# Kernel tuning notes

Measured on AMD Instinct MI355X. Metric: run time of the kernel, lower is better.

Reference implementation:

```python
import jax, jax.numpy as jnp
import numpy as np
from jax import lax

B, S, T = 512, 256, 10      # batch, src len, max_len (decoder steps)
V, E, H = 28, 32, 128       # vocab, embed, hidden
PAD = 0


def setup_inputs():
    key = jax.random.key(0)
    ks = jax.random.split(key, 16)
    k = 1.0 / np.sqrt(H)

    def u(kk, shape):
        return jax.random.uniform(kk, shape, jnp.float32, -k, k)

    embed = jax.random.normal(ks[0], (V, E), jnp.float32) * 0.02
    embed = embed.at[PAD].set(0.0)  # padding_idx=0 row is zero
    return dict(
        src=jax.random.randint(ks[1], (B, S), 0, V),
        target=jax.random.randint(ks[2], (B, T), 0, V),
        embed=embed,
        # PyTorch LSTM bias b = b_ih + b_hh folded into one vector (same math)
        enc_Wih_f=u(ks[3], (4 * H, E)), enc_Whh_f=u(ks[4], (4 * H, H)), enc_b_f=u(ks[5], (4 * H,)),
        enc_Wih_b=u(ks[6], (4 * H, E)), enc_Whh_b=u(ks[7], (4 * H, H)), enc_b_b=u(ks[8], (4 * H,)),
        dec_Wih=u(ks[9], (4 * H, E)), dec_Whh=u(ks[10], (4 * H, H)), dec_b=u(ks[11], (4 * H,)),
        proj_W=u(ks[12], (H, 2 * H)), proj_b=jnp.zeros((H,), jnp.float32),
        attn_W=u(ks[13], (H, 2 * H)), attn_b=jnp.zeros((H,), jnp.float32),
        out_W=u(ks[14], (V, H)), out_b=jnp.zeros((V,), jnp.float32),
    )


def _cell(h, c, xg, Whh):
    # PyTorch LSTMCell gate order: i, f, g, o
    g = xg + h @ Whh.T
    i, f, gg, o = jnp.split(g, 4, axis=-1)
    c = jax.nn.sigmoid(f) * c + jax.nn.sigmoid(i) * jnp.tanh(gg)
    return jax.nn.sigmoid(o) * jnp.tanh(c), c


def _run_lstm(x_emb, Wih, Whh, b):
    # precompute input projections for all steps: [S, B, 4H]
    xg = jnp.einsum('bse,ge->sbg', x_emb, Wih) + b
    h0 = jnp.zeros((x_emb.shape[0], Whh.shape[1]), x_emb.dtype)

    def step(carry, xg_t):
        h, c = _cell(carry[0], carry[1], xg_t, Whh)
        return (h, c), h

    (h, c), hs = lax.scan(step, (h0, h0), xg)
    return jnp.transpose(hs, (1, 0, 2)), h, c  # [B,S,H], [B,H], [B,H]


def _forward(src, target, embed, enc_Wih_f, enc_Whh_f, enc_b_f,
             enc_Wih_b, enc_Whh_b, enc_b_b, dec_Wih, dec_Whh, dec_b,
             proj_W, proj_b, attn_W, attn_b, out_W, out_b):
    src_emb = embed[src]  # [B,S,E]
    hs_f, hf, cf = _run_lstm(src_emb, enc_Wih_f, enc_Whh_f, enc_b_f)
    hs_r, hb, cb = _run_lstm(src_emb[:, ::-1], enc_Wih_b, enc_Whh_b, enc_b_b)
    enc_out = jnp.concatenate([hs_f, hs_r[:, ::-1]], axis=-1)  # [B,S,2H]
    h0, c0 = hf + hb, cf + cb  # sum over directions (num_layers=1)
    enc_proj = jnp.einsum('bsd,hd->bsh', enc_out, proj_W) + proj_b  # [B,S,H]

    # teacher forcing with ratio=1.0: decoder input tokens = [PAD, target[:, :-1]]
    dec_tok = jnp.concatenate(
        [jnp.full((src.shape[0], 1), PAD, target.dtype), target[:, :T - 1]], axis=1)
    xg_dec = jnp.einsum('bte,ge->tbg', embed[dec_tok], dec_Wih) + dec_b  # [T,B,4H]

    def dstep(carry, xg_t):
        h, c = _cell(carry[0], carry[1], xg_t, dec_Whh)
        scores = jnp.einsum('bsh,bh->bs', enc_proj, h)
        aw = jax.nn.softmax(scores, axis=1)
        ctx = jnp.einsum('bs,bsh->bh', aw, enc_proj)
        comb = jnp.tanh(jnp.concatenate([h, ctx], axis=1) @ attn_W.T + attn_b)
        logits = comb @ out_W.T + out_b
        return (h, c), logits

    _, logits = lax.scan(dstep, (h0, c0), xg_dec)  # [T,B,V]
    return jnp.transpose(logits, (1, 0, 2))  # [B,T,V]


def reference(src, target, embed, enc_Wih_f, enc_Whh_f, enc_b_f,
              enc_Wih_b, enc_Whh_b, enc_b_b, dec_Wih, dec_Whh, dec_b,
              proj_W, proj_b, attn_W, attn_b, out_W, out_b):
    return _forward(src, target, embed, enc_Wih_f, enc_Whh_f, enc_b_f,
                    enc_Wih_b, enc_Whh_b, enc_b_b, dec_Wih, dec_Whh, dec_b,
                    proj_W, proj_b, attn_W, attn_b, out_W, out_b)
```

## Files before the change

### kernel.cpp

```cpp
#include <hip/hip_runtime.h>
#include <hip/hip_bf16.h>
#include <stdint.h>

typedef unsigned short ushort_t;
typedef unsigned int uint_t;
typedef __attribute__((ext_vector_type(8))) short bfrag;
typedef __attribute__((ext_vector_type(4))) float f32x4;

#define B_ 512
#define S_ 256
#define T_ 10
#define V_ 28
#define H_ 128

#define XTD 0
#define XTG 14336
#define WTD 43008
#define AWT 108544
#define OWT 141312
#define PWT 144896
#define WPK 177664
#define HFIN 308736
#define CFIN 439808
#define HDEC 570880
#define HS_BYTE_OFF (1226240ull * 4ull)
#define PREP_N 308736

__device__ __forceinline__ float fast_exp2(float x) { return __builtin_amdgcn_exp2f(x); }
__device__ __forceinline__ float fast_rcp(float x)  { return __builtin_amdgcn_rcpf(x); }
__device__ __forceinline__ float sigm(float x) {
    return fast_rcp(1.f + fast_exp2(-1.4426950408889634f * x));
}
__device__ __forceinline__ float tanh_(float x) {
    return 1.f - 2.f * fast_rcp(1.f + fast_exp2(2.8853900817779268f * x));
}
__device__ __forceinline__ ushort_t f2bf(float x) {
    uint_t u = __float_as_uint(x);
    return (ushort_t)((u + 0x7FFFu + ((u >> 16) & 1u)) >> 16);
}
__device__ __forceinline__ float bflo(uint_t u) { return __uint_as_float(u << 16); }
__device__ __forceinline__ float bfhi(uint_t u) { return __uint_as_float(u & 0xFFFF0000u); }

__device__ __forceinline__ void lds_barrier() {
    asm volatile("s_waitcnt lgkmcnt(0)" ::: "memory");
    __builtin_amdgcn_s_barrier();
    __builtin_amdgcn_sched_barrier(0);
}

__global__ __launch_bounds__(256) void prep_kernel(
    const float* __restrict__ embed,
    const float* __restrict__ Wih_f, const float* __restrict__ b_f,
    const float* __restrict__ Wih_b, const float* __restrict__ b_b,
    const float* __restrict__ Wih_d, const float* __restrict__ b_d,
    const float* __restrict__ Whh_f, const float* __restrict__ Whh_b,
    const float* __restrict__ Whh_d,
    const float* __restrict__ attn_W, const float* __restrict__ out_W,
    const float* __restrict__ proj_W,
    float* __restrict__ ws)
{
    int i = blockIdx.x * 256 + threadIdx.x;
    if (i < XTG) {
        int v = i >> 9, jj = i & 511;
        float acc = b_d[jj];
        #pragma unroll
        for (int e = 0; e < 32; ++e) acc = fmaf(embed[v * 32 + e], Wih_d[jj * 32 + e], acc);
        ws[XTD + i] = acc;
    } else if (i < WTD) {
        int r = i - XTG; int d = r / 14336; int rem = r % 14336;
        int v = rem >> 9, q = rem & 511;
        int uu = q >> 2, g = q & 3;
        int jj = g * 128 + uu;
        const float* Wih = d ? Wih_b : Wih_f;
        const float* bb  = d ? b_b   : b_f;
        float acc = bb[jj];
        #pragma unroll
        for (int e = 0; e < 32; ++e) acc = fmaf(embed[v * 32 + e], Wih[jj * 32 + e], acc);
        ws[XTG + r] = acc;
    } else if (i < AWT) {
        int r = i - WTD; int k = r >> 9, jj = r & 511;
        ws[WTD + r] = Whh_d[jj * 128 + k];
    } else if (i < OWT) {
        int r = i - AWT; int k = r >> 7, uu = r & 127;
        ws[i] = attn_W[uu * 256 + k];
    } else if (i < PWT) {
        int r = i - OWT; int k = r / 28, v = r % 28;
        ws[i] = out_W[v * 128 + k];
    } else if (i < WPK) {
        int r = i - PWT; int k = r >> 7, uu = r & 127;
        ws[i] = proj_W[uu * 256 + k];
    } else if (i < PREP_N) {
        int i2 = (i - WPK) * 2;
        #pragma unroll
        for (int p = 0; p < 2; ++p, ++i2) {
            int e  = i2 & 7;
            int ll = (i2 >> 3) & 63;
            int kt = (i2 >> 9) & 3;
            int ni = (i2 >> 11) & 3;
            int wv = (i2 >> 13) & 7;
            int d  = (i2 >> 16) & 1;
            int jj = (ni * 8 + wv) * 16 + (ll & 15);
            int kp = kt * 32 + ((ll >> 4) << 3) + e;
            const float* Whh = d ? Whh_b : Whh_f;
            ((ushort_t*)(ws + WPK))[i2] = f2bf(Whh[jj * 128 + kp]);
        }
    }
}

__global__ __launch_bounds__(512, 2) void enc_kernel(
    const int* __restrict__ src,
    const float* __restrict__ xtg_base,
    const ushort_t* __restrict__ wpk,
    float* __restrict__ hfin, float* __restrict__ cfin,
    ushort_t* __restrict__ hs)
{
    const int bx = blockIdx.x;
    const int dir = bx >> 7;
    const int b0 = (bx & 127) << 2;
    const int tid = threadIdx.x;
    const int w = tid >> 6, l = tid & 63;
    const int lg = l >> 4, col = l & 15;
    const int u = (w << 4) + col;
    const int row = lg;

    __shared__ __align__(16) ushort_t hb[2][4][144];
    __shared__ __align__(16) int tokl[256][4];

    for (int i = tid; i < 1024; i += 512)
        tokl[i >> 2][i & 3] = src[(b0 + (i & 3)) * S_ + (i >> 2)];
    for (int i = tid; i < 576; i += 512) ((uint_t*)hb)[i] = 0u;

    const float* xtg = xtg_base + dir * 14336;

    bfrag bf[4][4];
    {
        const ushort_t* wb = wpk + (((size_t)dir * 8 + w) << 13) + l * 8;
        #pragma unroll
        for (int ni = 0; ni < 4; ++ni)
            #pragma unroll
            for (int kt = 0; kt < 4; ++kt)
                bf[ni][kt] = *reinterpret_cast<const bfrag*>(wb + ((ni * 4 + kt) << 9));
    }
    __syncthreads();

    float c_reg = 0.f, h_reg = 0.f;

    f32x4 xg_cur, xg_next;
    {
        int p0 = dir ? (S_ - 1) : 0;
        xg_cur = *reinterpret_cast<const f32x4*>(xtg + ((size_t)tokl[p0][row] << 9) + (u << 2));
    }

    const bfrag zf = {0, 0, 0, 0, 0, 0, 0, 0};
    bfrag af0 = zf, af1 = zf, af2 = zf, af3 = zf;
    const bool ard = ((col & 3) == 0);
    const int ar = col >> 2;
    const int swz = ar << 3;
    const f32x4 zacc = {0.f, 0.f, 0.f, 0.f};

    ushort_t* hs_ptr = hs + ((size_t)(b0 + row) * S_ + (dir ? (S_ - 1) : 0)) * 256
                          + dir * 128 + u;
    const int hs_step = dir ? -256 : 256;

    for (int t = 0; t < S_; ++t) {
        const int cb = t & 1, nb = cb ^ 1;

        if (t + 1 < S_) {
            int pn = dir ? (S_ - 2 - t) : (t + 1);
            xg_next = *reinterpret_cast<const f32x4*>(xtg + ((size_t)tokl[pn][row] << 9) + (u << 2));
        }

        if (ard) {
            const ushort_t* hp = &hb[cb][ar][0];
            af0 = *reinterpret_cast<const bfrag*>(hp + ((  0 + (lg << 3)) ^ swz));
            af1 = *reinterpret_cast<const bfrag*>(hp + (( 32 + (lg << 3)) ^ swz));
            af2 = *reinterpret_cast<const bfrag*>(hp + (( 64 + (lg << 3)) ^ swz));
            af3 = *reinterpret_cast<const bfrag*>(hp + (( 96 + (lg << 3)) ^ swz));
        }

        f32x4 a0 = __builtin_amdgcn_mfma_f32_16x16x32_bf16(af0, bf[0][0], zacc, 0, 0, 0);
        f32x4 a1 = __builtin_amdgcn_mfma_f32_16x16x32_bf16(af0, bf[1][0], zacc, 0, 0, 0);
        f32x4 a2 = __builtin_amdgcn_mfma_f32_16x16x32_bf16(af0, bf[2][0], zacc, 0, 0, 0);
        f32x4 a3 = __builtin_amdgcn_mfma_f32_16x16x32_bf16(af0, bf[3][0], zacc, 0, 0, 0);
        #define KT1(AF, kt) { \
            a0 = __builtin_amdgcn_mfma_f32_16x16x32_bf16(AF, bf[0][kt], a0, 0, 0, 0); \
            a1 = __builtin_amdgcn_mfma_f32_16x16x32_bf16(AF, bf[1][kt], a1, 0, 0, 0); \
            a2 = __builtin_amdgcn_mfma_f32_16x16x32_bf16(AF, bf[2][kt], a2, 0, 0, 0); \
            a3 = __builtin_amdgcn_mfma_f32_16x16x32_bf16(AF, bf[3][kt], a3, 0, 0, 0); \
        }
        KT1(af1, 1) KT1(af2, 2) KT1(af3, 3)
        #undef KT1

        {
            float gi = a0[0] + xg_cur[0], gf = a1[0] + xg_cur[1];
            float gg = a2[0] + xg_cur[2], go = a3[0] + xg_cur[3];
            float ii = sigm(gi), ff = sigm(gf), gG = tanh_(gg), oo = sigm(go);
            c_reg = ff * c_reg + ii * gG;
            float h = oo * tanh_(c_reg);
            h_reg = h;
            ushort_t hi = f2bf(h);
            hb[nb][row][u ^ (row << 3)] = hi;
            *hs_ptr = hi;
            hs_ptr += hs_step;
        }
        xg_cur = xg_next;
        lds_barrier();
    }

    hfin[dir * 65536 + (b0 + row) * 128 + u] = h_reg;
    cfin[dir * 65536 + (b0 + row) * 128 + u] = c_reg;
}

__global__ __launch_bounds__(512, 1) void dec_lstm_kernel(
    const int* __restrict__ target,
    const float* __restrict__ xt_d,
    const float* __restrict__ WhhT_d,
    const float* __restrict__ hfin, const float* __restrict__ cfin,
    float* __restrict__ hdec)
{
    const int b0 = blockIdx.x * 2;
    const int tid = threadIdx.x;
    const int j = tid;

    __shared__ __align__(16) float h_lds[2][128];
    __shared__ __align__(16) float g_lds[2][512];

    float4 w4[32];
    #pragma unroll
    for (int kc = 0; kc < 32; ++kc) {
        w4[kc].x = WhhT_d[(kc * 4 + 0) * 512 + j];
        w4[kc].y = WhhT_d[(kc * 4 + 1) * 512 + j];
        w4[kc].z = WhhT_d[(kc * 4 + 2) * 512 + j];
        w4[kc].w = WhhT_d[(kc * 4 + 3) * 512 + j];
    }
    const int r1 = tid >> 7, u1 = tid & 127;
    float c = 0.f;
    if (tid < 256) {
        int b = b0 + r1;
        c = cfin[b * 128 + u1] + cfin[65536 + b * 128 + u1];
        h_lds[r1][u1] = hfin[b * 128 + u1] + hfin[65536 + b * 128 + u1];
    }
    __syncthreads();

    for (int t = 0; t < T_; ++t) {
        int tok0 = (t == 0) ? 0 : target[(b0 + 0) * T_ + t - 1];
        int tok1 = (t == 0) ? 0 : target[(b0 + 1) * T_ + t - 1];
        float a0 = xt_d[tok0 * 512 + j];
        float a1 = xt_d[tok1 * 512 + j];
        #pragma unroll
        for (int kc = 0; kc < 32; ++kc) {
            const float4 w = w4[kc];
            const float4 h0 = *reinterpret_cast<const float4*>(&h_lds[0][kc * 4]);
            const float4 h1 = *reinterpret_cast<const float4*>(&h_lds[1][kc * 4]);
            a0 = fmaf(h0.x, w.x, a0); a0 = fmaf(h0.y, w.y, a0); a0 = fmaf(h0.z, w.z, a0); a0 = fmaf(h0.w, w.w, a0);
            a1 = fmaf(h1.x, w.x, a1); a1 = fmaf(h1.y, w.y, a1); a1 = fmaf(h1.z, w.z, a1); a1 = fmaf(h1.w, w.w, a1);
        }
        g_lds[0][j] = a0; g_lds[1][j] = a1;
        __syncthreads();
        if (tid < 256) {
            float gi = g_lds[r1][u1], gf = g_lds[r1][u1 + 128];
            float gg = g_lds[r1][u1 + 256], go = g_lds[r1][u1 + 384];
            float ii = sigm(gi), ff = sigm(gf), g_ = tanh_(gg), oo = sigm(go);
            c = ff * c + ii * g_;
            float h = oo * tanh_(c);
            h_lds[r1][u1] = h;
            hdec[((size_t)(b0 + r1) * T_ + t) * 128 + u1] = h;
        }
        __syncthreads();
    }
}

#define ESW(unit, row) ((((unit) ^ ((row) & 31))) << 3)
__global__ __launch_bounds__(512, 1) void attn_kernel(
    const float* __restrict__ hdec,
    const float* __restrict__ projW, const float* __restrict__ proj_b,
    const float* __restrict__ projWT,
    const float* __restrict__ attn_WT, const float* __restrict__ attn_b,
    const float* __restrict__ out_WT, const float* __restrict__ out_b,
    const ushort_t* __restrict__ hs, float* __restrict__ out)
{
    const int b = blockIdx.x;
    const int tid = threadIdx.x;

    __shared__ __align__(16) char smem[156672];
    ushort_t* e_lds = (ushort_t*)smem;
    float* hd   = (float*)(smem + 131072);
    float* q    = (float*)(smem + 136192);
    float* sc   = (float*)(smem + 146432);
    float* part = (float*)smem;
    float* wsum = (float*)(smem + 40960);

    const ushort_t* e = hs + (size_t)b * 65536;

    #pragma unroll 4
    for (int i = 0; i < 16; ++i) {
        int idx = i * 512 + tid;
        int row = idx >> 5, c = idx & 31;
        uint4 v = *reinterpret_cast<const uint4*>(e + idx * 8);
        *reinterpret_cast<uint4*>(e_lds + row * 256 + ESW(c, row)) = v;
    }
    for (int i = tid; i < 1280; i += 512) hd[i] = hdec[(size_t)b * 1280 + i];
    __syncthreads();

    {
        const int half = tid >> 8, d = tid & 255;
        float acc[5];
        #pragma unroll
        for (int i = 0; i < 5; ++i) acc[i] = 0.f;
        for (int k = 0; k < 128; ++k) {
            float pw = projW[k * 256 + d];
            #pragma unroll
            for (int i = 0; i < 5; ++i) acc[i] = fmaf(hd[(half * 5 + i) * 128 + k], pw, acc[i]);
        }
        int swd = d ^ ((((uint_t)d >> 5) & 7) << 2);
        #pragma unroll
        for (int i = 0; i < 5; ++i) q[(half * 5 + i) * 256 + swd] = acc[i];
    }
    __syncthreads();

    {
        const int w = tid >> 6, l = tid & 63;
        const int s3 = l >> 3, k8 = l & 7;
        for (int pass = 0; pass < 4; ++pass) {
            int s = w * 32 + pass * 8 + s3;
            const ushort_t* lrow = e_lds + s * 256;
            uint4 e0 = *reinterpret_cast<const uint4*>(lrow + ESW((k8 << 2) + 0, s));
            uint4 e1 = *reinterpret_cast<const uint4*>(lrow + ESW((k8 << 2) + 1, s));
            uint4 e2 = *reinterpret_cast<const uint4*>(lrow + ESW((k8 << 2) + 2, s));
            uint4 e3 = *reinterpret_cast<const uint4*>(lrow + ESW((k8 << 2) + 3, s));
            float acc[10];
            #pragma unroll
            for (int t = 0; t < 10; ++t) {
                const float* qb = &q[t * 256];
                float a = 0.f;
                #define QCH(i) (*reinterpret_cast<const float4*>(&qb[(k8 * 32 + (i) * 4) ^ (k8 << 2)]))
                #define DOT4(pa, pb, qv) { float4 q_ = (qv); \
                    a = fmaf(bflo(pa), q_.x, a); a = fmaf(bfhi(pa), q_.y, a); \
                    a = fmaf(bflo(pb), q_.z, a); a = fmaf(bfhi(pb), q_.w, a); }
                DOT4(e0.x, e0.y, QCH(0)); DOT4(e0.z, e0.w, QCH(1));
                DOT4(e1.x, e1.y, QCH(2)); DOT4(e1.z, e1.w, QCH(3));
                DOT4(e2.x, e2.y, QCH(4)); DOT4(e2.z, e2.w, QCH(5));
                DOT4(e3.x, e3.y, QCH(6)); DOT4(e3.z, e3.w, QCH(7));
                #undef QCH
                #undef DOT4
                acc[t] = a;
            }
            #pragma unroll
            for (int t = 0; t < 10; ++t) {
                acc[t] += __shfl_xor(acc[t], 1);
                acc[t] += __shfl_xor(acc[t], 2);
                acc[t] += __shfl_xor(acc[t], 4);
            }
            if (k8 == 0) {
                #pragma unroll
                for (int t = 0; t < 10; ++t) sc[t * 256 + s] = acc[t];
            }
        }
    }
    __syncthreads();

    {
        const int w = tid >> 6, l = tid & 63;
        for (int t = w; t < 10; t += 8) {
            float4 sv = *reinterpret_cast<const float4*>(&sc[t * 256 + l * 4]);
            float m = fmaxf(fmaxf(sv.x, sv.y), fmaxf(sv.z, sv.w));
            #pragma unroll
            for (int o = 1; o < 64; o <<= 1) m = fmaxf(m, __shfl_xor(m, o));
            float e0 = fast_exp2((sv.x - m) * 1.4426950408889634f);
            float e1 = fast_exp2((sv.y - m) * 1.4426950408889634f);
            float e2 = fast_exp2((sv.z - m) * 1.4426950408889634f);
            float e3 = fast_exp2((sv.w - m) * 1.4426950408889634f);
            float ssum = e0 + e1 + e2 + e3;
            #pragma unroll
            for (int o = 1; o < 64; o <<= 1) ssum += __shfl_xor(ssum, o);
            float inv = fast_rcp(ssum);
            *reinterpret_cast<float4*>(&sc[t * 256 + l * 4]) =
                make_float4(e0 * inv, e1 * inv, e2 * inv, e3 * inv);
        }
    }
    __syncthreads();

    {
        const int w = tid >> 6, l = tid & 63;
        const int chunk = w >> 1, tH = (w & 1) * 5;
        const int unit = l >> 1, half = (l & 1) << 2;
        float ax[5], ay[5], az[5], aw2[5];
        #pragma unroll
        for (int i = 0; i < 5; ++i) { ax[i] = 0.f; ay[i] = 0.f; az[i] = 0.f; aw2[i] = 0.f; }
        for (int s = chunk * 64; s < chunk * 64 + 64; ++s) {
            uint2 uu = *reinterpret_cast<const uint2*>(e_lds + s * 256 + ESW(unit, s) + half);
            float v0 = bflo(uu.x), v1 = bfhi(uu.x), v2 = bflo(uu.y), v3 = bfhi(uu.y);
            #pragma unroll
            for (int i = 0; i < 5; ++i) {
                float awv = sc[(tH + i) * 256 + s];
                ax[i] = fmaf(v0, awv, ax[i]); ay[i] = fmaf(v1, awv, ay[i]);
                az[i] = fmaf(v2, awv, az[i]); aw2[i] = fmaf(v3, awv, aw2[i]);
            }
        }
        __syncthreads();
        #pragma unroll
        for (int i = 0; i < 5; ++i)
            *reinterpret_cast<float4*>(&part[(chunk * 10 + tH + i) * 256 + l * 4]) =
                make_float4(ax[i], ay[i], az[i], aw2[i]);
    }
    __syncthreads();

    for (int i = tid; i < 2560; i += 512)
        wsum[i] = part[i] + part[2560 + i] + part[5120 + i] + part[7680 + i];
    if (tid < 512) wsum[2560 + tid] = 0.f;
    __syncthreads();

    {
        const int u = tid & 127, th = tid >> 7;
        const int st = (th < 2) ? th * 3 : 6 + (th - 2) * 2;
        const int cn = (th < 2) ? 3 : 2;
        float acc[3];
        #pragma unroll
        for (int i = 0; i < 3; ++i) acc[i] = proj_b[u];
        for (int k = 0; k < 256; ++k) {
            float pw = projWT[k * 128 + u];
            #pragma unroll
            for (int i = 0; i < 3; ++i) acc[i] = fmaf(pw, wsum[(st + i) * 256 + k], acc[i]);
        }
        #pragma unroll
        for (int i = 0; i < 3; ++i)
            if (i < cn) q[(st + i) * 128 + u] = acc[i];
    }
    __syncthreads();

    {
        const int u = tid & 127, th = tid >> 7;
        const int st = (th < 2) ? th * 3 : 6 + (th - 2) * 2;
        const int cn = (th < 2) ? 3 : 2;
        float acc[3];
        #pragma unroll
        for (int i = 0; i < 3; ++i) acc[i] = attn_b[u];
        for (int k = 0; k < 128; ++k) {
            float a1 = attn_WT[k * 128 + u];
            #pragma unroll
            for (int i = 0; i < 3; ++i) {
                int tt = (st + i < 10) ? (st + i) : 9;
                acc[i] = fmaf(a1, hd[tt * 128 + k], acc[i]);
            }
        }
        for (int k = 0; k < 128; ++k) {
            float a2 = attn_WT[(128 + k) * 128 + u];
            #pragma unroll
            for (int i = 0; i < 3; ++i) {
                int tt = (st + i < 10) ? (st + i) : 9;
                acc[i] = fmaf(a2, q[tt * 128 + k], acc[i]);
            }
        }
        #pragma unroll
        for (int i = 0; i < 3; ++i)
            if (i < cn) q[1280 + (st + i) * 128 + u] = tanh_(acc[i]);
    }
    __syncthreads();

    for (int o = tid; o < 280; o += 512) {
        int t = o / 28, v = o - t * 28;
        float acc = out_b[v];
        #pragma unroll 4
        for (int k = 0; k < 128; ++k)
            acc = fmaf(out_WT[k * 28 + v], q[1280 + t * 128 + k], acc);
        out[(size_t)b * 280 + o] = acc;
    }
}

extern "C" void kernel_launch(void* const* d_in, const int* in_sizes, int n_in,
                              void* d_out, int out_size, void* d_ws, size_t ws_size,
                              hipStream_t stream) {
    const int* src      = (const int*)d_in[0];
    const int* target   = (const int*)d_in[1];
    const float* embed  = (const float*)d_in[2];
    const float* Wih_f  = (const float*)d_in[3];
    const float* Whh_f  = (const float*)d_in[4];
    const float* b_f    = (const float*)d_in[5];
    const float* Wih_b  = (const float*)d_in[6];
    const float* Whh_b  = (const float*)d_in[7];
    const float* b_b    = (const float*)d_in[8];
    const float* Wih_d  = (const float*)d_in[9];
    const float* Whh_d  = (const float*)d_in[10];
    const float* b_d    = (const float*)d_in[11];
    const float* proj_W = (const float*)d_in[12];
    const float* proj_b = (const float*)d_in[13];
    const float* attn_W = (const float*)d_in[14];
    const float* attn_b = (const float*)d_in[15];
    const float* out_W  = (const float*)d_in[16];
    const float* out_b  = (const float*)d_in[17];

    float* ws = (float*)d_ws;
    ushort_t* hs = (ushort_t*)((char*)d_ws + HS_BYTE_OFF);
    float* out = (float*)d_out;

    prep_kernel<<<(PREP_N + 255) / 256, 256, 0, stream>>>(
        embed, Wih_f, b_f, Wih_b, b_b, Wih_d, b_d,
        Whh_f, Whh_b, Whh_d, attn_W, out_W, proj_W, ws);

    enc_kernel<<<256, 512, 0, stream>>>(
        src, ws + XTG, (const ushort_t*)(ws + WPK),
        ws + HFIN, ws + CFIN, hs);

    dec_lstm_kernel<<<256, 512, 0, stream>>>(
        target, ws + XTD, ws + WTD, ws + HFIN, ws + CFIN, ws + HDEC);

    attn_kernel<<<512, 512, 0, stream>>>(
        ws + HDEC, proj_W, proj_b, ws + PWT, ws + AWT, attn_b,
        ws + OWT, out_b, hs, out);
}
```

Baseline: 280.6 us.

## Run decoder LSTM on bf16 MFMA and prefetch encoder states in attention

The decoder LSTM now uses the same bf16 MFMA path as the encoder. Its Whh is packed in prep into fragment layout, each block handles four batch rows, and gate inputs are laid out interleaved per unit so one float4 load fetches all four gates. The attention kernel issues all global loads of encoder states before computing the query projection, so load latency overlaps with compute. It also hoists the per-timestep q loads out of the score loop and unrolls the context accumulation by four source positions. The decoder's precision drops from fp32 to bf16 weights and hidden state, and prep relies on the ws region beyond WPK being large enough for the extra packed weights.

```diff
diff --git a/kernel.cpp b/kernel.cpp
--- a/kernel.cpp
+++ b/kernel.cpp
@@ -60,7 +60,9 @@
 {
     int i = blockIdx.x * 256 + threadIdx.x;
     if (i < XTG) {
-        int v = i >> 9, jj = i & 511;
+        int v = i >> 9, q = i & 511;
+        int uu = q >> 2, g = q & 3;
+        int jj = g * 128 + uu;
         float acc = b_d[jj];
         #pragma unroll
         for (int e = 0; e < 32; ++e) acc = fmaf(embed[v * 32 + e], Wih_d[jj * 32 + e], acc);
@@ -77,8 +79,7 @@
         for (int e = 0; e < 32; ++e) acc = fmaf(embed[v * 32 + e], Wih[jj * 32 + e], acc);
         ws[XTG + r] = acc;
     } else if (i < AWT) {
-        int r = i - WTD; int k = r >> 9, jj = r & 511;
-        ws[WTD + r] = Whh_d[jj * 128 + k];
+        ws[i] = 0.f;
     } else if (i < OWT) {
         int r = i - AWT; int k = r >> 7, uu = r & 127;
         ws[i] = attn_W[uu * 256 + k];
@@ -88,20 +89,32 @@
     } else if (i < WPK) {
         int r = i - PWT; int k = r >> 7, uu = r & 127;
         ws[i] = proj_W[uu * 256 + k];
-    } else if (i < PREP_N) {
+    } else {
         int i2 = (i - WPK) * 2;
         #pragma unroll
         for (int p = 0; p < 2; ++p, ++i2) {
-            int e  = i2 & 7;
-            int ll = (i2 >> 3) & 63;
-            int kt = (i2 >> 9) & 3;
-            int ni = (i2 >> 11) & 3;
-            int wv = (i2 >> 13) & 7;
-            int d  = (i2 >> 16) & 1;
-            int jj = (ni * 8 + wv) * 16 + (ll & 15);
-            int kp = kt * 32 + ((ll >> 4) << 3) + e;
-            const float* Whh = d ? Whh_b : Whh_f;
-            ((ushort_t*)(ws + WPK))[i2] = f2bf(Whh[jj * 128 + kp]);
+            if (i2 < 131072) {
+                int e  = i2 & 7;
+                int ll = (i2 >> 3) & 63;
+                int kt = (i2 >> 9) & 3;
+                int ni = (i2 >> 11) & 3;
+                int wv = (i2 >> 13) & 7;
+                int d  = (i2 >> 16) & 1;
+                int jj = (ni * 8 + wv) * 16 + (ll & 15);
+                int kp = kt * 32 + ((ll >> 4) << 3) + e;
+                const float* Whh = d ? Whh_b : Whh_f;
+                ((ushort_t*)(ws + WPK))[i2] = f2bf(Whh[jj * 128 + kp]);
+            } else if (i2 < 196608) {
+                int j2 = i2 - 131072;
+                int e  = j2 & 7;
+                int ll = (j2 >> 3) & 63;
+                int kt = (j2 >> 9) & 3;
+                int ni = (j2 >> 11) & 3;
+                int wv = (j2 >> 13) & 7;
+                int jj = (ni * 8 + wv) * 16 + (ll & 15);
+                int kp = kt * 32 + ((ll >> 4) << 3) + e;
+                ((ushort_t*)(ws + WPK))[i2] = f2bf(Whh_d[jj * 128 + kp]);
+            }
         }
     }
 }
@@ -210,62 +223,92 @@
     cfin[dir * 65536 + (b0 + row) * 128 + u] = c_reg;
 }
 
-__global__ __launch_bounds__(512, 1) void dec_lstm_kernel(
+__global__ __launch_bounds__(512, 2) void dec_kernel(
     const int* __restrict__ target,
-    const float* __restrict__ xt_d,
-    const float* __restrict__ WhhT_d,
+    const float* __restrict__ xtd_gi,
+    const ushort_t* __restrict__ wpk,
     const float* __restrict__ hfin, const float* __restrict__ cfin,
     float* __restrict__ hdec)
 {
-    const int b0 = blockIdx.x * 2;
+    const int b0 = blockIdx.x << 2;
     const int tid = threadIdx.x;
-    const int j = tid;
-
-    __shared__ __align__(16) float h_lds[2][128];
-    __shared__ __align__(16) float g_lds[2][512];
-
-    float4 w4[32];
-    #pragma unroll
-    for (int kc = 0; kc < 32; ++kc) {
-        w4[kc].x = WhhT_d[(kc * 4 + 0) * 512 + j];
-        w4[kc].y = WhhT_d[(kc * 4 + 1) * 512 + j];
-        w4[kc].z = WhhT_d[(kc * 4 + 2) * 512 + j];
-        w4[kc].w = WhhT_d[(kc * 4 + 3) * 512 + j];
-    }
-    const int r1 = tid >> 7, u1 = tid & 127;
-    float c = 0.f;
-    if (tid < 256) {
-        int b = b0 + r1;
-        c = cfin[b * 128 + u1] + cfin[65536 + b * 128 + u1];
-        h_lds[r1][u1] = hfin[b * 128 + u1] + hfin[65536 + b * 128 + u1];
-    }
-    __syncthreads();
+    const int w = tid >> 6, l = tid & 63;
+    const int lg = l >> 4, col = l & 15;
+    const int u = (w << 4) + col;
+    const int row = lg;
+
+    __shared__ __align__(16) ushort_t hb[2][4][144];
+    __shared__ __align__(16) int tokl[T_][4];
+
+    if (tid < 40) {
+        int t = tid >> 2, r = tid & 3;
+        tokl[t][r] = (t == 0) ? 0 : target[(b0 + r) * T_ + t - 1];
+    }
+
+    bfrag bf[4][4];
+    {
+        const ushort_t* wb = wpk + 131072 + ((size_t)w << 13) + l * 8;
+        #pragma unroll
+        for (int ni = 0; ni < 4; ++ni)
+            #pragma unroll
+            for (int kt = 0; kt < 4; ++kt)
+                bf[ni][kt] = *reinterpret_cast<const bfrag*>(wb + ((ni * 4 + kt) << 9));
+    }
+
+    float c_reg, h_reg;
+    {
+        int gb = (b0 + row) * 128 + u;
+        h_reg = hfin[gb] + hfin[65536 + gb];
+        c_reg = cfin[gb] + cfin[65536 + gb];
+        hb[0][row][u ^ (row << 3)] = f2bf(h_reg);
+    }
+    __syncthreads();
+
+    const bfrag zf = {0, 0, 0, 0, 0, 0, 0, 0};
+    bfrag af0 = zf, af1 = zf, af2 = zf, af3 = zf;
+    const bool ard = ((col & 3) == 0);
+    const int ar = col >> 2;
+    const int swz = ar << 3;
+    const f32x4 zacc = {0.f, 0.f, 0.f, 0.f};
 
     for (int t = 0; t < T_; ++t) {
-        int tok0 = (t == 0) ? 0 : target[(b0 + 0) * T_ + t - 1];
-        int tok1 = (t == 0) ? 0 : target[(b0 + 1) * T_ + t - 1];
-        float a0 = xt_d[tok0 * 512 + j];
-        float a1 = xt_d[tok1 * 512 + j];
-        #pragma unroll
-        for (int kc = 0; kc < 32; ++kc) {
-            const float4 w = w4[kc];
-            const float4 h0 = *reinterpret_cast<const float4*>(&h_lds[0][kc * 4]);
-            const float4 h1 = *reinterpret_cast<const float4*>(&h_lds[1][kc * 4]);
-            a0 = fmaf(h0.x, w.x, a0); a0 = fmaf(h0.y, w.y, a0); a0 = fmaf(h0.z, w.z, a0); a0 = fmaf(h0.w, w.w, a0);
-            a1 = fmaf(h1.x, w.x, a1); a1 = fmaf(h1.y, w.y, a1); a1 = fmaf(h1.z, w.z, a1); a1 = fmaf(h1.w, w.w, a1);
-        }
-        g_lds[0][j] = a0; g_lds[1][j] = a1;
-        __syncthreads();
-        if (tid < 256) {
-            float gi = g_lds[r1][u1], gf = g_lds[r1][u1 + 128];
-            float gg = g_lds[r1][u1 + 256], go = g_lds[r1][u1 + 384];
-            float ii = sigm(gi), ff = sigm(gf), g_ = tanh_(gg), oo = sigm(go);
-            c = ff * c + ii * g_;
-            float h = oo * tanh_(c);
-            h_lds[r1][u1] = h;
-            hdec[((size_t)(b0 + r1) * T_ + t) * 128 + u1] = h;
-        }
-        __syncthreads();
+        const int cb = t & 1, nb = cb ^ 1;
+
+        f32x4 xgc = *reinterpret_cast<const f32x4*>(
+            xtd_gi + ((size_t)tokl[t][row] << 9) + (u << 2));
+
+        if (ard) {
+            const ushort_t* hp = &hb[cb][ar][0];
+            af0 = *reinterpret_cast<const bfrag*>(hp + ((  0 + (lg << 3)) ^ swz));
+            af1 = *reinterpret_cast<const bfrag*>(hp + (( 32 + (lg << 3)) ^ swz));
+            af2 = *reinterpret_cast<const bfrag*>(hp + (( 64 + (lg << 3)) ^ swz));
+            af3 = *reinterpret_cast<const bfrag*>(hp + (( 96 + (lg << 3)) ^ swz));
+        }
+
+        f32x4 a0 = __builtin_amdgcn_mfma_f32_16x16x32_bf16(af0, bf[0][0], zacc, 0, 0, 0);
+        f32x4 a1 = __builtin_amdgcn_mfma_f32_16x16x32_bf16(af0, bf[1][0], zacc, 0, 0, 0);
+        f32x4 a2 = __builtin_amdgcn_mfma_f32_16x16x32_bf16(af0, bf[2][0], zacc, 0, 0, 0);
+        f32x4 a3 = __builtin_amdgcn_mfma_f32_16x16x32_bf16(af0, bf[3][0], zacc, 0, 0, 0);
+        #define KT1(AF, kt) { \
+            a0 = __builtin_amdgcn_mfma_f32_16x16x32_bf16(AF, bf[0][kt], a0, 0, 0, 0); \
+            a1 = __builtin_amdgcn_mfma_f32_16x16x32_bf16(AF, bf[1][kt], a1, 0, 0, 0); \
+            a2 = __builtin_amdgcn_mfma_f32_16x16x32_bf16(AF, bf[2][kt], a2, 0, 0, 0); \
+            a3 = __builtin_amdgcn_mfma_f32_16x16x32_bf16(AF, bf[3][kt], a3, 0, 0, 0); \
+        }
+        KT1(af1, 1) KT1(af2, 2) KT1(af3, 3)
+        #undef KT1
+
+        {
+            float gi = a0[0] + xgc[0], gf = a1[0] + xgc[1];
+            float gg = a2[0] + xgc[2], go = a3[0] + xgc[3];
+            float ii = sigm(gi), ff = sigm(gf), gG = tanh_(gg), oo = sigm(go);
+            c_reg = ff * c_reg + ii * gG;
+            float h = oo * tanh_(c_reg);
+            h_reg = h;
+            hb[nb][row][u ^ (row << 3)] = f2bf(h);
+            hdec[((size_t)(b0 + row) * T_ + t) * 128 + u] = h;
+        }
+        lds_barrier();
     }
 }
 
@@ -291,68 +334,71 @@
 
     const ushort_t* e = hs + (size_t)b * 65536;
 
-    #pragma unroll 4
+    uint4 st[16];
+    #pragma unroll
+    for (int i = 0; i < 16; ++i)
+        st[i] = *reinterpret_cast<const uint4*>(e + (i * 512 + tid) * 8);
+
+    for (int i = tid; i < 1280; i += 512) hd[i] = hdec[(size_t)b * 1280 + i];
+    lds_barrier();
+
+    {
+        const int half = tid >> 8, d = tid & 255;
+        float acc[5];
+        #pragma unroll
+        for (int i = 0; i < 5; ++i) acc[i] = 0.f;
+        for (int k = 0; k < 128; ++k) {
+            float pw = projW[k * 256 + d];
+            #pragma unroll
+            for (int i = 0; i < 5; ++i) acc[i] = fmaf(hd[(half * 5 + i) * 128 + k], pw, acc[i]);
+        }
+        int swd = d ^ ((((uint_t)d >> 5) & 7) << 2);
+        #pragma unroll
+        for (int i = 0; i < 5; ++i) q[(half * 5 + i) * 256 + swd] = acc[i];
+    }
+
+    #pragma unroll
     for (int i = 0; i < 16; ++i) {
         int idx = i * 512 + tid;
         int row = idx >> 5, c = idx & 31;
-        uint4 v = *reinterpret_cast<const uint4*>(e + idx * 8);
-        *reinterpret_cast<uint4*>(e_lds + row * 256 + ESW(c, row)) = v;
-    }
-    for (int i = tid; i < 1280; i += 512) hd[i] = hdec[(size_t)b * 1280 + i];
-    __syncthreads();
-
-    {
-        const int half = tid >> 8, d = tid & 255;
-        float acc[5];
-        #pragma unroll
-        for (int i = 0; i < 5; ++i) acc[i] = 0.f;
-        for (int k = 0; k < 128; ++k) {
-            float pw = projW[k * 256 + d];
-            #pragma unroll
-            for (int i = 0; i < 5; ++i) acc[i] = fmaf(hd[(half * 5 + i) * 128 + k], pw, acc[i]);
-        }
-        int swd = d ^ ((((uint_t)d >> 5) & 7) << 2);
-        #pragma unroll
-        for (int i = 0; i < 5; ++i) q[(half * 5 + i) * 256 + swd] = acc[i];
-    }
-    __syncthreads();
+        *reinterpret_cast<uint4*>(e_lds + row * 256 + ESW(c, row)) = st[i];
+    }
+    lds_barrier();
 
     {
         const int w = tid >> 6, l = tid & 63;
         const int s3 = l >> 3, k8 = l & 7;
-        for (int pass = 0; pass < 4; ++pass) {
-            int s = w * 32 + pass * 8 + s3;
+        uint4 E0[4], E1[4], E2[4], E3[4];
+        #pragma unroll
+        for (int p = 0; p < 4; ++p) {
+            int s = w * 32 + p * 8 + s3;
             const ushort_t* lrow = e_lds + s * 256;
-            uint4 e0 = *reinterpret_cast<const uint4*>(lrow + ESW((k8 << 2) + 0, s));
-            uint4 e1 = *reinterpret_cast<const uint4*>(lrow + ESW((k8 << 2) + 1, s));
-            uint4 e2 = *reinterpret_cast<const uint4*>(lrow + ESW((k8 << 2) + 2, s));
-            uint4 e3 = *reinterpret_cast<const uint4*>(lrow + ESW((k8 << 2) + 3, s));
-            float acc[10];
-            #pragma unroll
-            for (int t = 0; t < 10; ++t) {
-                const float* qb = &q[t * 256];
+            E0[p] = *reinterpret_cast<const uint4*>(lrow + ESW((k8 << 2) + 0, s));
+            E1[p] = *reinterpret_cast<const uint4*>(lrow + ESW((k8 << 2) + 1, s));
+            E2[p] = *reinterpret_cast<const uint4*>(lrow + ESW((k8 << 2) + 2, s));
+            E3[p] = *reinterpret_cast<const uint4*>(lrow + ESW((k8 << 2) + 3, s));
+        }
+        for (int t = 0; t < 10; ++t) {
+            const float* qb = &q[t * 256];
+            #define QCH(i) (*reinterpret_cast<const float4*>(&qb[(k8 * 32 + (i) * 4) ^ (k8 << 2)]))
+            float4 Q0 = QCH(0), Q1 = QCH(1), Q2 = QCH(2), Q3 = QCH(3);
+            float4 Q4 = QCH(4), Q5 = QCH(5), Q6 = QCH(6), Q7 = QCH(7);
+            #undef QCH
+            #pragma unroll
+            for (int p = 0; p < 4; ++p) {
                 float a = 0.f;
-                #define QCH(i) (*reinterpret_cast<const float4*>(&qb[(k8 * 32 + (i) * 4) ^ (k8 << 2)]))
                 #define DOT4(pa, pb, qv) { float4 q_ = (qv); \
                     a = fmaf(bflo(pa), q_.x, a); a = fmaf(bfhi(pa), q_.y, a); \
                     a = fmaf(bflo(pb), q_.z, a); a = fmaf(bfhi(pb), q_.w, a); }
-                DOT4(e0.x, e0.y, QCH(0)); DOT4(e0.z, e0.w, QCH(1));
-                DOT4(e1.x, e1.y, QCH(2)); DOT4(e1.z, e1.w, QCH(3));
-                DOT4(e2.x, e2.y, QCH(4)); DOT4(e2.z, e2.w, QCH(5));
-                DOT4(e3.x, e3.y, QCH(6)); DOT4(e3.z, e3.w, QCH(7));
-                #undef QCH
+                DOT4(E0[p].x, E0[p].y, Q0); DOT4(E0[p].z, E0[p].w, Q1);
+                DOT4(E1[p].x, E1[p].y, Q2); DOT4(E1[p].z, E1[p].w, Q3);
+                DOT4(E2[p].x, E2[p].y, Q4); DOT4(E2[p].z, E2[p].w, Q5);
+                DOT4(E3[p].x, E3[p].y, Q6); DOT4(E3[p].z, E3[p].w, Q7);
                 #undef DOT4
-                acc[t] = a;
-            }
-            #pragma unroll
-            for (int t = 0; t < 10; ++t) {
-                acc[t] += __shfl_xor(acc[t], 1);
-                acc[t] += __shfl_xor(acc[t], 2);
-                acc[t] += __shfl_xor(acc[t], 4);
-            }
-            if (k8 == 0) {
-                #pragma unroll
-                for (int t = 0; t < 10; ++t) sc[t * 256 + s] = acc[t];
+                a += __shfl_xor(a, 1);
+                a += __shfl_xor(a, 2);
+                a += __shfl_xor(a, 4);
+                if (k8 == 0) sc[t * 256 + (w * 32 + p * 8 + s3)] = a;
             }
         }
     }
@@ -382,18 +428,28 @@
     {
         const int w = tid >> 6, l = tid & 63;
         const int chunk = w >> 1, tH = (w & 1) * 5;
-        const int unit = l >> 1, half = (l & 1) << 2;
+        const int sbase = chunk * 64;
+        const int unit = l >> 1, half2 = (l & 1) << 2;
         float ax[5], ay[5], az[5], aw2[5];
         #pragma unroll
         for (int i = 0; i < 5; ++i) { ax[i] = 0.f; ay[i] = 0.f; az[i] = 0.f; aw2[i] = 0.f; }
-        for (int s = chunk * 64; s < chunk * 64 + 64; ++s) {
-            uint2 uu = *reinterpret_cast<const uint2*>(e_lds + s * 256 + ESW(unit, s) + half);
-            float v0 = bflo(uu.x), v1 = bfhi(uu.x), v2 = bflo(uu.y), v3 = bfhi(uu.y);
+        for (int c4 = 0; c4 < 16; ++c4) {
+            int s0 = sbase + c4 * 4;
+            uint2 eA = *reinterpret_cast<const uint2*>(e_lds + (s0 + 0) * 256 + ESW(unit, s0 + 0) + half2);
+            uint2 eB = *reinterpret_cast<const uint2*>(e_lds + (s0 + 1) * 256 + ESW(unit, s0 + 1) + half2);
+            uint2 eC = *reinterpret_cast<const uint2*>(e_lds + (s0 + 2) * 256 + ESW(unit, s0 + 2) + half2);
+            uint2 eD = *reinterpret_cast<const uint2*>(e_lds + (s0 + 3) * 256 + ESW(unit, s0 + 3) + half2);
             #pragma unroll
             for (int i = 0; i < 5; ++i) {
-                float awv = sc[(tH + i) * 256 + s];
-                ax[i] = fmaf(v0, awv, ax[i]); ay[i] = fmaf(v1, awv, ay[i]);
-                az[i] = fmaf(v2, awv, az[i]); aw2[i] = fmaf(v3, awv, aw2[i]);
+                float4 a4 = *reinterpret_cast<const float4*>(&sc[(tH + i) * 256 + s0]);
+                ax[i]  = fmaf(bflo(eA.x), a4.x, ax[i]);  ay[i]  = fmaf(bfhi(eA.x), a4.x, ay[i]);
+                az[i]  = fmaf(bflo(eA.y), a4.x, az[i]);  aw2[i] = fmaf(bfhi(eA.y), a4.x, aw2[i]);
+                ax[i]  = fmaf(bflo(eB.x), a4.y, ax[i]);  ay[i]  = fmaf(bfhi(eB.x), a4.y, ay[i]);
+                az[i]  = fmaf(bflo(eB.y), a4.y, az[i]);  aw2[i] = fmaf(bfhi(eB.y), a4.y, aw2[i]);
+                ax[i]  = fmaf(bflo(eC.x), a4.z, ax[i]);  ay[i]  = fmaf(bfhi(eC.x), a4.z, ay[i]);
+                az[i]  = fmaf(bflo(eC.y), a4.z, az[i]);  aw2[i] = fmaf(bfhi(eC.y), a4.z, aw2[i]);
+                ax[i]  = fmaf(bflo(eD.x), a4.w, ax[i]);  ay[i]  = fmaf(bfhi(eD.x), a4.w, ay[i]);
+                az[i]  = fmaf(bflo(eD.y), a4.w, az[i]);  aw2[i] = fmaf(bfhi(eD.y), a4.w, aw2[i]);
             }
         }
         __syncthreads();
@@ -411,7 +467,7 @@
 
     {
         const int u = tid & 127, th = tid >> 7;
-        const int st = (th < 2) ? th * 3 : 6 + (th - 2) * 2;
+        const int st5 = (th < 2) ? th * 3 : 6 + (th - 2) * 2;
         const int cn = (th < 2) ? 3 : 2;
         float acc[3];
         #pragma unroll
@@ -419,17 +475,17 @@
         for (int k = 0; k < 256; ++k) {
             float pw = projWT[k * 128 + u];
             #pragma unroll
-            for (int i = 0; i < 3; ++i) acc[i] = fmaf(pw, wsum[(st + i) * 256 + k], acc[i]);
+            for (int i = 0; i < 3; ++i) acc[i] = fmaf(pw, wsum[(st5 + i) * 256 + k], acc[i]);
         }
         #pragma unroll
         for (int i = 0; i < 3; ++i)
-            if (i < cn) q[(st + i) * 128 + u] = acc[i];
+            if (i < cn) q[(st5 + i) * 128 + u] = acc[i];
     }
     __syncthreads();
 
     {
         const int u = tid & 127, th = tid >> 7;
-        const int st = (th < 2) ? th * 3 : 6 + (th - 2) * 2;
+        const int st6 = (th < 2) ? th * 3 : 6 + (th - 2) * 2;
         const int cn = (th < 2) ? 3 : 2;
         float acc[3];
         #pragma unroll
@@ -438,7 +494,7 @@
             float a1 = attn_WT[k * 128 + u];
             #pragma unroll
             for (int i = 0; i < 3; ++i) {
-                int tt = (st + i < 10) ? (st + i) : 9;
+                int tt = (st6 + i < 10) ? (st6 + i) : 9;
                 acc[i] = fmaf(a1, hd[tt * 128 + k], acc[i]);
             }
         }
@@ -446,13 +502,13 @@
             float a2 = attn_WT[(128 + k) * 128 + u];
             #pragma unroll
             for (int i = 0; i < 3; ++i) {
-                int tt = (st + i < 10) ? (st + i) : 9;
+                int tt = (st6 + i < 10) ? (st6 + i) : 9;
                 acc[i] = fmaf(a2, q[tt * 128 + k], acc[i]);
             }
         }
         #pragma unroll
         for (int i = 0; i < 3; ++i)
-            if (i < cn) q[1280 + (st + i) * 128 + u] = tanh_(acc[i]);
+            if (i < cn) q[1280 + (st6 + i) * 128 + u] = tanh_(acc[i]);
     }
     __syncthreads();
 
@@ -500,8 +556,9 @@
         src, ws + XTG, (const ushort_t*)(ws + WPK),
         ws + HFIN, ws + CFIN, hs);
 
-    dec_lstm_kernel<<<256, 512, 0, stream>>>(
-        target, ws + XTD, ws + WTD, ws + HFIN, ws + CFIN, ws + HDEC);
+    dec_kernel<<<128, 512, 0, stream>>>(
+        target, ws + XTD, (const ushort_t*)(ws + WPK),
+        ws + HFIN, ws + CFIN, ws + HDEC);
 
     attn_kernel<<<512, 512, 0, stream>>>(
         ws + HDEC, proj_W, proj_b, ws + PWT, ws + AWT, attn_b,
```

New measurement: 264.6 us. 1.06x faster.
